# Kernel tuning notes

Measured on AMD Instinct MI355X. Metric: run time of the kernel, lower is better.

## Reference

```python
import jax, jax.numpy as jnp
import numpy as np

N_NODES = 50000
N_EDGES = 1600000
N_GRAPHS = 256
IN_CH = 128
HID = 128
OUT_CH = 10


def gcn_conv(x, W, b, src, dst, ew, num_nodes):
    # PyG GCNConv: add self-loops (weight 1), symmetric deg^-1/2 normalization,
    # linear transform first, aggregate via scatter-add, bias after.
    loop = jnp.arange(num_nodes)
    s = jnp.concatenate([src, loop])
    d = jnp.concatenate([dst, loop])
    w = jnp.concatenate([ew, jnp.ones((num_nodes,), x.dtype)])
    deg = jax.ops.segment_sum(w, d, num_segments=num_nodes)
    dinv = jnp.where(deg > 0, jax.lax.rsqrt(deg), 0.0)
    norm = dinv[s] * dinv[d] * w                     # [E+N]
    h = x @ W                                        # [N, H]
    msg = h[s] * norm[:, None]                       # gather + scale
    out = jax.ops.segment_sum(msg, d, num_segments=num_nodes)  # scatter-add
    return out + b


def setup_inputs() -> dict:
    key = jax.random.key(0)
    ks = jax.random.split(key, 12)
    x = jax.random.normal(ks[0], (N_NODES, IN_CH), jnp.float32)
    edge_index = jax.random.randint(ks[1], (2, N_EDGES), 0, N_NODES, jnp.int64)
    edge_weight = jax.random.uniform(ks[2], (N_EDGES,), jnp.float32)
    batch = jnp.sort(jax.random.randint(ks[3], (N_NODES,), 0, N_GRAPHS, jnp.int64))
    s = 1.0 / np.sqrt(HID)
    W1 = jax.random.normal(ks[4], (IN_CH, HID), jnp.float32) / np.sqrt(IN_CH)
    b1 = jnp.zeros((HID,), jnp.float32)
    W2 = jax.random.normal(ks[5], (HID, HID), jnp.float32) * s
    b2 = jnp.zeros((HID,), jnp.float32)
    W3 = jax.random.normal(ks[6], (HID, HID), jnp.float32) * s
    b3 = jnp.zeros((HID,), jnp.float32)
    lw1 = jax.random.normal(ks[7], (HID, HID), jnp.float32) * s
    lb1 = jax.random.normal(ks[8], (HID,), jnp.float32) * s
    lw2 = jax.random.normal(ks[9], (HID, OUT_CH), jnp.float32) * s
    lb2 = jax.random.normal(ks[10], (OUT_CH,), jnp.float32) * s
    return {"x": x, "edge_index": edge_index, "edge_weight": edge_weight,
            "batch": batch, "W1": W1, "b1": b1, "W2": W2, "b2": b2,
            "W3": W3, "b3": b3, "lw1": lw1, "lb1": lb1, "lw2": lw2, "lb2": lb2}


def reference(x, edge_index, edge_weight, batch, W1, b1, W2, b2, W3, b3, lw1, lb1, lw2, lb2):
    src, dst = edge_index[0], edge_index[1]
    h = jax.nn.relu(gcn_conv(x, W1, b1, src, dst, edge_weight, N_NODES))
    h = jax.nn.relu(gcn_conv(h, W2, b2, src, dst, edge_weight, N_NODES))
    h = gcn_conv(h, W3, b3, src, dst, edge_weight, N_NODES)
    # global mean pool over graphs
    sums = jax.ops.segment_sum(h, batch, num_segments=N_GRAPHS)
    cnt = jax.ops.segment_sum(jnp.ones((N_NODES,), h.dtype), batch, num_segments=N_GRAPHS)
    emb = sums / jnp.maximum(cnt, 1.0)[:, None]      # [G, HID]
    out = (emb @ lw1 + lb1) @ lw2 + lb2              # classify: lin1 -> lin2
    return out
```

## Files before the change

### kernel.cpp

```cpp
#include <hip/hip_runtime.h>

#define N_NODES 50000
#define N_EDGES 1600000
#define N_GRAPHS 256
#define HID 128
#define OUT_CH 10
#define NBUCK 512
#define BNODES ((N_NODES + NBUCK - 1) / NBUCK)
#define BCAP 6144
#define P1BLK 250
#define EPB (N_EDGES / P1BLK)
#define DSENTINEL 127
#define NR 4
#define RSTEP ((N_NODES + NR - 1) / NR)
#define PAD_R 40

typedef __bf16 bf16x8 __attribute__((ext_vector_type(8)));
typedef float f32x4 __attribute__((ext_vector_type(4)));

__device__ inline unsigned bf16rne(float f) {
    unsigned u = __float_as_uint(f);
    return (u + 0x7fffu + ((u >> 16) & 1u)) >> 16;
}

__global__ __launch_bounds__(1024) void bucket_k(const int* __restrict__ src,
                                                 const int* __restrict__ dst,
                                                 const float* __restrict__ ew,
                                                 int* __restrict__ bcount,
                                                 int2* __restrict__ cpair) {
    __shared__ int hist[NBUCK];
    __shared__ int base[NBUCK];
    int t = threadIdx.x;
    for (int i = t; i < NBUCK; i += 1024) hist[i] = 0;
    __syncthreads();
    const int ch0 = blockIdx.x * (EPB / 4);
    const int ch1 = ch0 + (EPB / 4);
    const int4* dst4 = (const int4*)dst;
    for (int ci = ch0 + t; ci < ch1; ci += 1024) {
        int4 d4 = dst4[ci];
        atomicAdd(&hist[d4.x / BNODES], 1);
        atomicAdd(&hist[d4.y / BNODES], 1);
        atomicAdd(&hist[d4.z / BNODES], 1);
        atomicAdd(&hist[d4.w / BNODES], 1);
    }
    __syncthreads();
    for (int i = t; i < NBUCK; i += 1024) {
        int c = hist[i];
        base[i] = (c > 0) ? atomicAdd(&bcount[i], (c + 7) & ~7) : 0;
        hist[i] = 0;
    }
    __syncthreads();
    for (int ci = ch0 + t; ci < ch1; ci += 1024) {
        int4 d4 = dst4[ci];
        int e = ci * 4;
#define PROC(dd, ee)                                              \
        {                                                         \
            int b = (dd) / BNODES;                                \
            int off = base[b] + atomicAdd(&hist[b], 1);           \
            if (off < BCAP) {                                     \
                int2 p;                                           \
                p.x = (((dd) - b * BNODES) << 16) | src[ee];      \
                p.y = __float_as_int(ew[ee]);                     \
                cpair[b * BCAP + off] = p;                        \
            }                                                     \
        }
        PROC(d4.x, e)
        PROC(d4.y, e + 1)
        PROC(d4.z, e + 2)
        PROC(d4.w, e + 3)
#undef PROC
    }
    __syncthreads();
    for (int i = t; i < NBUCK; i += 1024) {
        int c = hist[i];
        int ac = (c + 7) & ~7;
        for (int j = c; j < ac; ++j) {
            int off = base[i] + j;
            if (off < BCAP) {
                int2 p;
                p.x = DSENTINEL << 16;
                p.y = 0;
                cpair[i * BCAP + off] = p;
            }
        }
    }
}

__global__ __launch_bounds__(512) void ell_scatter_k(const int* __restrict__ bcount,
                                                     const int2* __restrict__ cpair,
                                                     int2* __restrict__ ell,
                                                     unsigned* __restrict__ fill4,
                                                     float* __restrict__ dinv) {
    __shared__ int lfill[BNODES * NR];
    __shared__ float wsum[BNODES];
    int b = blockIdx.x;
    int t = threadIdx.x;
    for (int i = t; i < BNODES * NR; i += 512) lfill[i] = 0;
    for (int i = t; i < BNODES; i += 512) wsum[i] = 0.f;
    __syncthreads();
    int cnt = bcount[b];
    if (cnt > BCAP) cnt = BCAP;
    int n0 = b * BNODES;
    int sbase = b * BCAP;
    for (int i = t; i < cnt; i += 512) {
        int2 p = cpair[sbase + i];
        int dloc = p.x >> 16;
        if (dloc < BNODES) {
            int s = p.x & 0xffff;
            int r = s / RSTEP;
            int pos = atomicAdd(&lfill[dloc * NR + r], 1);
            atomicAdd(&wsum[dloc], __int_as_float(p.y));
            if (pos < PAD_R) {
                int2 q;
                q.x = s;
                q.y = p.y;
                ell[((size_t)(n0 + dloc) * NR + r) * PAD_R + pos] = q;
            }
        }
    }
    __syncthreads();
    for (int i = t; i < BNODES; i += 512) {
        int n = n0 + i;
        if (n < N_NODES) {
            unsigned f = 0;
#pragma unroll
            for (int r = 0; r < NR; ++r) {
                int c = lfill[i * NR + r];
                if (c > PAD_R) c = PAD_R;
                f |= (unsigned)c << (8 * r);
            }
            fill4[n] = f;
            dinv[n] = rsqrtf(wsum[i] + 1.0f);
        }
    }
}

__global__ __launch_bounds__(256) void prep_k(const int* __restrict__ batch,
                                              int* __restrict__ gstart,
                                              const float* __restrict__ W1,
                                              const float* __restrict__ W2,
                                              const float* __restrict__ W3,
                                              unsigned short* __restrict__ Wt) {
    int idx = blockIdx.x * 256 + threadIdx.x;
    if (idx < 3 * 16384) {
        int m = idx >> 14;
        int r = idx & 16383;
        const float* W = (m == 0) ? W1 : (m == 1) ? W2 : W3;
        int c = r >> 7, k = r & 127;
        Wt[idx] = (unsigned short)bf16rne(W[k * 128 + c]);
    }
    if (idx < N_NODES) {
        int b = batch[idx];
        int bprev = (idx == 0) ? -1 : batch[idx - 1];
        for (int g = bprev + 1; g <= b; ++g) gstart[g] = idx;
        if (idx == N_NODES - 1) {
            for (int g = b + 1; g <= N_GRAPHS; ++g) gstart[g] = N_NODES;
        }
    }
}

__global__ __launch_bounds__(256) void gemm_mfma_k(const float* __restrict__ A32,
                                                   const unsigned short* __restrict__ Ab,
                                                   const unsigned short* __restrict__ Wt,
                                                   unsigned short* __restrict__ Cb,
                                                   int n_rows) {
    int tid = threadIdx.x;
    int wave = tid >> 6;
    int lane = tid & 63;
    int m = lane & 15;
    int quad = lane >> 4;
    int row = blockIdx.x * 64 + wave * 16 + m;
    int rowc = row < n_rows ? row : n_rows - 1;
    f32x4 acc[8] = {};
#pragma unroll
    for (int kc = 0; kc < 4; ++kc) {
        bf16x8 a;
        if (A32) {
            const float4* Ar = (const float4*)(A32 + (size_t)rowc * 128 + kc * 32 + quad * 8);
            float4 lo = Ar[0], hi = Ar[1];
            union { bf16x8 v; unsigned short s[8]; } u;
            u.s[0] = (unsigned short)bf16rne(lo.x);
            u.s[1] = (unsigned short)bf16rne(lo.y);
            u.s[2] = (unsigned short)bf16rne(lo.z);
            u.s[3] = (unsigned short)bf16rne(lo.w);
            u.s[4] = (unsigned short)bf16rne(hi.x);
            u.s[5] = (unsigned short)bf16rne(hi.y);
            u.s[6] = (unsigned short)bf16rne(hi.z);
            u.s[7] = (unsigned short)bf16rne(hi.w);
            a = u.v;
        } else {
            a = *(const bf16x8*)(Ab + (size_t)rowc * 128 + kc * 32 + quad * 8);
        }
#pragma unroll
        for (int ct = 0; ct < 8; ++ct) {
            bf16x8 b = *(const bf16x8*)(Wt + (size_t)(ct * 16 + m) * 128 + kc * 32 + quad * 8);
            acc[ct] = __builtin_amdgcn_mfma_f32_16x16x32_bf16(a, b, acc[ct], 0, 0, 0);
        }
    }
    int obase = blockIdx.x * 64 + wave * 16 + quad * 4;
#pragma unroll
    for (int ct = 0; ct < 8; ++ct) {
#pragma unroll
        for (int r = 0; r < 4; ++r) {
            int n = obase + r;
            if (n < n_rows)
                Cb[(size_t)n * 128 + ct * 16 + m] = (unsigned short)bf16rne(acc[ct][r]);
        }
    }
}

__global__ __launch_bounds__(256) void agg_k(const unsigned short* __restrict__ tb,
                                             const unsigned* __restrict__ fill4,
                                             const int2* __restrict__ ell,
                                             const float* __restrict__ dinv,
                                             const float* __restrict__ bias,
                                             unsigned short* __restrict__ outB, int relu) {
    int lane = threadIdx.x & 15;
    int local = threadIdx.x >> 4;
    int n = blockIdx.x * 16 + local;
    if (n >= N_NODES) return;
    float dn = dinv[n];
#define UNP(q, f)                                                 \
    float f##0 = __uint_as_float((q).x << 16);                    \
    float f##1 = __uint_as_float((q).x & 0xffff0000u);            \
    float f##2 = __uint_as_float((q).y << 16);                    \
    float f##3 = __uint_as_float((q).y & 0xffff0000u);            \
    float f##4 = __uint_as_float((q).z << 16);                    \
    float f##5 = __uint_as_float((q).z & 0xffff0000u);            \
    float f##6 = __uint_as_float((q).w << 16);                    \
    float f##7 = __uint_as_float((q).w & 0xffff0000u);
    uint4 qs = ((const uint4*)(tb + (size_t)n * 128))[lane];
    UNP(qs, s)
    float acc0 = s0 * dn, acc1 = s1 * dn, acc2 = s2 * dn, acc3 = s3 * dn;
    float acc4 = s4 * dn, acc5 = s5 * dn, acc6 = s6 * dn, acc7 = s7 * dn;
    unsigned f4 = fill4[n];
#pragma unroll
    for (int r = 0; r < NR; ++r) {
        int c = (f4 >> (8 * r)) & 255;
        const int2* ep = ell + ((size_t)n * NR + r) * PAD_R;
        int i = 0;
        for (; i + 4 <= c; i += 4) {
            int2 p0 = ep[i], p1 = ep[i + 1], p2 = ep[i + 2], p3 = ep[i + 3];
            uint4 q0 = ((const uint4*)(tb + (size_t)p0.x * 128))[lane];
            uint4 q1 = ((const uint4*)(tb + (size_t)p1.x * 128))[lane];
            uint4 q2 = ((const uint4*)(tb + (size_t)p2.x * 128))[lane];
            uint4 q3 = ((const uint4*)(tb + (size_t)p3.x * 128))[lane];
            float w0 = __int_as_float(p0.y) * dinv[p0.x];
            float w1 = __int_as_float(p1.y) * dinv[p1.x];
            float w2 = __int_as_float(p2.y) * dinv[p2.x];
            float w3 = __int_as_float(p3.y) * dinv[p3.x];
            UNP(q0, a)
            UNP(q1, b)
            UNP(q2, cc)
            UNP(q3, d)
            acc0 += a0 * w0 + b0 * w1 + cc0 * w2 + d0 * w3;
            acc1 += a1 * w0 + b1 * w1 + cc1 * w2 + d1 * w3;
            acc2 += a2 * w0 + b2 * w1 + cc2 * w2 + d2 * w3;
            acc3 += a3 * w0 + b3 * w1 + cc3 * w2 + d3 * w3;
            acc4 += a4 * w0 + b4 * w1 + cc4 * w2 + d4 * w3;
            acc5 += a5 * w0 + b5 * w1 + cc5 * w2 + d5 * w3;
            acc6 += a6 * w0 + b6 * w1 + cc6 * w2 + d6 * w3;
            acc7 += a7 * w0 + b7 * w1 + cc7 * w2 + d7 * w3;
        }
        for (; i < c; ++i) {
            int2 p = ep[i];
            float w = __int_as_float(p.y) * dinv[p.x];
            uint4 q = ((const uint4*)(tb + (size_t)p.x * 128))[lane];
            UNP(q, a)
            acc0 += a0 * w; acc1 += a1 * w; acc2 += a2 * w; acc3 += a3 * w;
            acc4 += a4 * w; acc5 += a5 * w; acc6 += a6 * w; acc7 += a7 * w;
        }
    }
#undef UNP
    float4 b0 = ((const float4*)bias)[lane * 2];
    float4 b1 = ((const float4*)bias)[lane * 2 + 1];
    acc0 = acc0 * dn + b0.x; acc1 = acc1 * dn + b0.y;
    acc2 = acc2 * dn + b0.z; acc3 = acc3 * dn + b0.w;
    acc4 = acc4 * dn + b1.x; acc5 = acc5 * dn + b1.y;
    acc6 = acc6 * dn + b1.z; acc7 = acc7 * dn + b1.w;
    if (relu) {
        acc0 = fmaxf(acc0, 0.f); acc1 = fmaxf(acc1, 0.f);
        acc2 = fmaxf(acc2, 0.f); acc3 = fmaxf(acc3, 0.f);
        acc4 = fmaxf(acc4, 0.f); acc5 = fmaxf(acc5, 0.f);
        acc6 = fmaxf(acc6, 0.f); acc7 = fmaxf(acc7, 0.f);
    }
    uint4 pk;
    pk.x = bf16rne(acc0) | (bf16rne(acc1) << 16);
    pk.y = bf16rne(acc2) | (bf16rne(acc3) << 16);
    pk.z = bf16rne(acc4) | (bf16rne(acc5) << 16);
    pk.w = bf16rne(acc6) | (bf16rne(acc7) << 16);
    ((uint4*)(outB + (size_t)n * 128))[lane] = pk;
}

#define PCHUNK 49
__global__ __launch_bounds__(128) void pool1_k(const unsigned short* __restrict__ hb,
                                               const int* __restrict__ batch,
                                               float* __restrict__ pool) {
    int c = threadIdx.x;
    int n0 = blockIdx.x * PCHUNK;
    if (n0 >= N_NODES) return;
    int n1 = n0 + PCHUNK;
    if (n1 > N_NODES) n1 = N_NODES;
    int g = batch[n0];
    float run = 0.f;
    for (int n = n0; n < n1; ++n) {
        int gn = batch[n];
        if (gn != g) {
            atomicAdd(&pool[g * 128 + c], run);
            run = 0.f;
            g = gn;
        }
        run += __uint_as_float((unsigned)hb[(size_t)n * 128 + c] << 16);
    }
    atomicAdd(&pool[g * 128 + c], run);
}

__global__ __launch_bounds__(128) void cls2_k(const float* __restrict__ pool,
                                              const int* __restrict__ gstart,
                                              const float* __restrict__ lw1,
                                              const float* __restrict__ lb1,
                                              const float* __restrict__ lw2,
                                              const float* __restrict__ lb2,
                                              float* __restrict__ out) {
    __shared__ float emb[128];
    __shared__ float mid[128];
    int g = blockIdx.x, c = threadIdx.x;
    float cntf = fmaxf((float)(gstart[g + 1] - gstart[g]), 1.0f);
    emb[c] = pool[(size_t)g * 128 + c] / cntf;
    __syncthreads();
    float a = lb1[c];
    for (int k = 0; k < 128; ++k) a += emb[k] * lw1[k * 128 + c];
    mid[c] = a;
    __syncthreads();
    if (c < OUT_CH) {
        float o = lb2[c];
        for (int k = 0; k < 128; ++k) o += mid[k] * lw2[k * OUT_CH + c];
        out[g * OUT_CH + c] = o;
    }
}

extern "C" void kernel_launch(void* const* d_in, const int* in_sizes, int n_in,
                              void* d_out, int out_size, void* d_ws, size_t ws_size,
                              hipStream_t stream) {
    const float* x = (const float*)d_in[0];
    const int* ei = (const int*)d_in[1];
    const int* src = ei;
    const int* dst = ei + N_EDGES;
    const float* ew = (const float*)d_in[2];
    const int* batch = (const int*)d_in[3];
    const float* W1 = (const float*)d_in[4];
    const float* b1 = (const float*)d_in[5];
    const float* W2 = (const float*)d_in[6];
    const float* b2 = (const float*)d_in[7];
    const float* W3 = (const float*)d_in[8];
    const float* b3 = (const float*)d_in[9];
    const float* lw1 = (const float*)d_in[10];
    const float* lb1 = (const float*)d_in[11];
    const float* lw2 = (const float*)d_in[12];
    const float* lb2 = (const float*)d_in[13];
    float* out = (float*)d_out;

    char* ws = (char*)d_ws;
    size_t off = 0;
    auto alloc = [&](size_t bytes) {
        size_t cur = off;
        off += (bytes + 255) & ~(size_t)255;
        return cur;
    };
    size_t o_bcount = alloc(NBUCK * 4);
    size_t o_pool = alloc(N_GRAPHS * HID * 4);
    size_t zero_end = off;
    size_t o_fill4 = alloc(N_NODES * 4);
    size_t o_dinv = alloc(N_NODES * 4);
    size_t o_gstart = alloc((N_GRAPHS + 1) * 4);
    size_t o_wt = alloc(3 * 16384 * 2);
    size_t o_ell = alloc((size_t)N_NODES * NR * PAD_R * 8);
    size_t o_cpair = alloc((size_t)NBUCK * BCAP * 8);
    size_t o_gAb = alloc((size_t)N_NODES * HID * 2);
    size_t o_aggB = alloc((size_t)N_NODES * HID * 2);
    (void)ws_size;

    int* bcount = (int*)(ws + o_bcount);
    float* pool = (float*)(ws + o_pool);
    unsigned* fill4 = (unsigned*)(ws + o_fill4);
    float* dinv = (float*)(ws + o_dinv);
    int* gstart = (int*)(ws + o_gstart);
    unsigned short* Wt = (unsigned short*)(ws + o_wt);
    int2* ell = (int2*)(ws + o_ell);
    int2* cpair = (int2*)(ws + o_cpair);
    unsigned short* gAb = (unsigned short*)(ws + o_gAb);
    unsigned short* aggB = (unsigned short*)(ws + o_aggB);

    hipMemsetAsync(d_ws, 0, zero_end, stream);

    bucket_k<<<P1BLK, 1024, 0, stream>>>(src, dst, ew, bcount, cpair);
    ell_scatter_k<<<NBUCK, 512, 0, stream>>>(bcount, cpair, ell, fill4, dinv);
    prep_k<<<196, 256, 0, stream>>>(batch, gstart, W1, W2, W3, Wt);

    int gemm_blocks = (N_NODES + 63) / 64;
    int agg_blocks = (N_NODES + 15) / 16;
    gemm_mfma_k<<<gemm_blocks, 256, 0, stream>>>(x, (const unsigned short*)0, Wt, gAb, N_NODES);
    agg_k<<<agg_blocks, 256, 0, stream>>>(gAb, fill4, ell, dinv, b1, aggB, 1);
    gemm_mfma_k<<<gemm_blocks, 256, 0, stream>>>((const float*)0, aggB, Wt + 16384, gAb, N_NODES);
    agg_k<<<agg_blocks, 256, 0, stream>>>(gAb, fill4, ell, dinv, b2, aggB, 1);
    gemm_mfma_k<<<gemm_blocks, 256, 0, stream>>>((const float*)0, aggB, Wt + 32768, gAb, N_NODES);
    agg_k<<<agg_blocks, 256, 0, stream>>>(gAb, fill4, ell, dinv, b3, aggB, 0);

    pool1_k<<<(N_NODES + PCHUNK - 1) / PCHUNK, 128, 0, stream>>>(aggB, batch, pool);
    cls2_k<<<N_GRAPHS, 128, 0, stream>>>(pool, gstart, lw1, lb1, lw2, lb2, out);
}
```

Measured before the change: 392.0 us.

## Aggregate before transform and fuse GEMM into aggregation kernel

Reorders each GCN layer to aggregate the raw features first and then apply the weight matrix, using linearity (A·X·W = (A·X)·W). The GEMM is fused into the aggregation kernel through a shared-memory tile and MFMA, and a separate kernel converts x to bf16 once. This drops three standalone GEMM launches and the round trip of the intermediate feature matrix through global memory. In exchange the rounding order changes: features are rounded to bf16 after aggregation instead of after the transform. The fused kernel also carries extra shared-memory and register pressure under a 6-block occupancy hint.

```diff
diff --git a/kernel.cpp b/kernel.cpp
--- a/kernel.cpp
+++ b/kernel.cpp
@@ -159,66 +159,32 @@
     }
 }
 
-__global__ __launch_bounds__(256) void gemm_mfma_k(const float* __restrict__ A32,
-                                                   const unsigned short* __restrict__ Ab,
+__global__ __launch_bounds__(256) void xconv_k(const float* __restrict__ x,
+                                               unsigned short* __restrict__ xb) {
+    int i = blockIdx.x * 256 + threadIdx.x;
+    if (i >= N_NODES * 16) return;
+    const float4* p = (const float4*)x + (size_t)i * 2;
+    float4 lo = p[0], hi = p[1];
+    uint4 pk;
+    pk.x = bf16rne(lo.x) | (bf16rne(lo.y) << 16);
+    pk.y = bf16rne(lo.z) | (bf16rne(lo.w) << 16);
+    pk.z = bf16rne(hi.x) | (bf16rne(hi.y) << 16);
+    pk.w = bf16rne(hi.z) | (bf16rne(hi.w) << 16);
+    ((uint4*)xb)[i] = pk;
+}
+
+__global__ __launch_bounds__(256, 6) void aggemm_k(const unsigned short* __restrict__ tb,
+                                                   const unsigned* __restrict__ fill4,
+                                                   const int2* __restrict__ ell,
+                                                   const float* __restrict__ dinv,
                                                    const unsigned short* __restrict__ Wt,
-                                                   unsigned short* __restrict__ Cb,
-                                                   int n_rows) {
-    int tid = threadIdx.x;
-    int wave = tid >> 6;
-    int lane = tid & 63;
-    int m = lane & 15;
-    int quad = lane >> 4;
-    int row = blockIdx.x * 64 + wave * 16 + m;
-    int rowc = row < n_rows ? row : n_rows - 1;
-    f32x4 acc[8] = {};
-#pragma unroll
-    for (int kc = 0; kc < 4; ++kc) {
-        bf16x8 a;
-        if (A32) {
-            const float4* Ar = (const float4*)(A32 + (size_t)rowc * 128 + kc * 32 + quad * 8);
-            float4 lo = Ar[0], hi = Ar[1];
-            union { bf16x8 v; unsigned short s[8]; } u;
-            u.s[0] = (unsigned short)bf16rne(lo.x);
-            u.s[1] = (unsigned short)bf16rne(lo.y);
-            u.s[2] = (unsigned short)bf16rne(lo.z);
-            u.s[3] = (unsigned short)bf16rne(lo.w);
-            u.s[4] = (unsigned short)bf16rne(hi.x);
-            u.s[5] = (unsigned short)bf16rne(hi.y);
-            u.s[6] = (unsigned short)bf16rne(hi.z);
-            u.s[7] = (unsigned short)bf16rne(hi.w);
-            a = u.v;
-        } else {
-            a = *(const bf16x8*)(Ab + (size_t)rowc * 128 + kc * 32 + quad * 8);
-        }
-#pragma unroll
-        for (int ct = 0; ct < 8; ++ct) {
-            bf16x8 b = *(const bf16x8*)(Wt + (size_t)(ct * 16 + m) * 128 + kc * 32 + quad * 8);
-            acc[ct] = __builtin_amdgcn_mfma_f32_16x16x32_bf16(a, b, acc[ct], 0, 0, 0);
-        }
-    }
-    int obase = blockIdx.x * 64 + wave * 16 + quad * 4;
-#pragma unroll
-    for (int ct = 0; ct < 8; ++ct) {
-#pragma unroll
-        for (int r = 0; r < 4; ++r) {
-            int n = obase + r;
-            if (n < n_rows)
-                Cb[(size_t)n * 128 + ct * 16 + m] = (unsigned short)bf16rne(acc[ct][r]);
-        }
-    }
-}
-
-__global__ __launch_bounds__(256) void agg_k(const unsigned short* __restrict__ tb,
-                                             const unsigned* __restrict__ fill4,
-                                             const int2* __restrict__ ell,
-                                             const float* __restrict__ dinv,
-                                             const float* __restrict__ bias,
-                                             unsigned short* __restrict__ outB, int relu) {
-    int lane = threadIdx.x & 15;
+                                                   const float* __restrict__ bias,
+                                                   unsigned short* __restrict__ outB,
+                                                   int relu) {
+    __shared__ unsigned short tile[16][136];
+    int lane16 = threadIdx.x & 15;
     int local = threadIdx.x >> 4;
     int n = blockIdx.x * 16 + local;
-    if (n >= N_NODES) return;
     float dn = dinv[n];
 #define UNP(q, f)                                                 \
     float f##0 = __uint_as_float((q).x << 16);                    \
@@ -229,7 +195,7 @@
     float f##5 = __uint_as_float((q).z & 0xffff0000u);            \
     float f##6 = __uint_as_float((q).w << 16);                    \
     float f##7 = __uint_as_float((q).w & 0xffff0000u);
-    uint4 qs = ((const uint4*)(tb + (size_t)n * 128))[lane];
+    uint4 qs = ((const uint4*)(tb + (size_t)n * 128))[lane16];
     UNP(qs, s)
     float acc0 = s0 * dn, acc1 = s1 * dn, acc2 = s2 * dn, acc3 = s3 * dn;
     float acc4 = s4 * dn, acc5 = s5 * dn, acc6 = s6 * dn, acc7 = s7 * dn;
@@ -241,10 +207,10 @@
         int i = 0;
         for (; i + 4 <= c; i += 4) {
             int2 p0 = ep[i], p1 = ep[i + 1], p2 = ep[i + 2], p3 = ep[i + 3];
-            uint4 q0 = ((const uint4*)(tb + (size_t)p0.x * 128))[lane];
-            uint4 q1 = ((const uint4*)(tb + (size_t)p1.x * 128))[lane];
-            uint4 q2 = ((const uint4*)(tb + (size_t)p2.x * 128))[lane];
-            uint4 q3 = ((const uint4*)(tb + (size_t)p3.x * 128))[lane];
+            uint4 q0 = ((const uint4*)(tb + (size_t)p0.x * 128))[lane16];
+            uint4 q1 = ((const uint4*)(tb + (size_t)p1.x * 128))[lane16];
+            uint4 q2 = ((const uint4*)(tb + (size_t)p2.x * 128))[lane16];
+            uint4 q3 = ((const uint4*)(tb + (size_t)p3.x * 128))[lane16];
             float w0 = __int_as_float(p0.y) * dinv[p0.x];
             float w1 = __int_as_float(p1.y) * dinv[p1.x];
             float w2 = __int_as_float(p2.y) * dinv[p2.x];
@@ -265,31 +231,50 @@
         for (; i < c; ++i) {
             int2 p = ep[i];
             float w = __int_as_float(p.y) * dinv[p.x];
-            uint4 q = ((const uint4*)(tb + (size_t)p.x * 128))[lane];
+            uint4 q = ((const uint4*)(tb + (size_t)p.x * 128))[lane16];
             UNP(q, a)
             acc0 += a0 * w; acc1 += a1 * w; acc2 += a2 * w; acc3 += a3 * w;
             acc4 += a4 * w; acc5 += a5 * w; acc6 += a6 * w; acc7 += a7 * w;
         }
     }
 #undef UNP
-    float4 b0 = ((const float4*)bias)[lane * 2];
-    float4 b1 = ((const float4*)bias)[lane * 2 + 1];
-    acc0 = acc0 * dn + b0.x; acc1 = acc1 * dn + b0.y;
-    acc2 = acc2 * dn + b0.z; acc3 = acc3 * dn + b0.w;
-    acc4 = acc4 * dn + b1.x; acc5 = acc5 * dn + b1.y;
-    acc6 = acc6 * dn + b1.z; acc7 = acc7 * dn + b1.w;
-    if (relu) {
-        acc0 = fmaxf(acc0, 0.f); acc1 = fmaxf(acc1, 0.f);
-        acc2 = fmaxf(acc2, 0.f); acc3 = fmaxf(acc3, 0.f);
-        acc4 = fmaxf(acc4, 0.f); acc5 = fmaxf(acc5, 0.f);
-        acc6 = fmaxf(acc6, 0.f); acc7 = fmaxf(acc7, 0.f);
-    }
+    acc0 *= dn; acc1 *= dn; acc2 *= dn; acc3 *= dn;
+    acc4 *= dn; acc5 *= dn; acc6 *= dn; acc7 *= dn;
     uint4 pk;
     pk.x = bf16rne(acc0) | (bf16rne(acc1) << 16);
     pk.y = bf16rne(acc2) | (bf16rne(acc3) << 16);
     pk.z = bf16rne(acc4) | (bf16rne(acc5) << 16);
     pk.w = bf16rne(acc6) | (bf16rne(acc7) << 16);
-    ((uint4*)(outB + (size_t)n * 128))[lane] = pk;
+    *(uint4*)&tile[local][lane16 * 8] = pk;
+    __syncthreads();
+
+    int wave = threadIdx.x >> 6;
+    int lane = threadIdx.x & 63;
+    int m = lane & 15;
+    int quad = lane >> 4;
+    f32x4 acc[2] = {};
+#pragma unroll
+    for (int kc = 0; kc < 4; ++kc) {
+        bf16x8 a = *(const bf16x8*)&tile[m][kc * 32 + quad * 8];
+#pragma unroll
+        for (int ctl = 0; ctl < 2; ++ctl) {
+            int ct = wave * 2 + ctl;
+            bf16x8 bfr = *(const bf16x8*)(Wt + (size_t)(ct * 16 + m) * 128 + kc * 32 + quad * 8);
+            acc[ctl] = __builtin_amdgcn_mfma_f32_16x16x32_bf16(a, bfr, acc[ctl], 0, 0, 0);
+        }
+    }
+#pragma unroll
+    for (int ctl = 0; ctl < 2; ++ctl) {
+        int col = (wave * 2 + ctl) * 16 + m;
+        float bv = bias[col];
+#pragma unroll
+        for (int r = 0; r < 4; ++r) {
+            int nr = blockIdx.x * 16 + quad * 4 + r;
+            float v = acc[ctl][r] + bv;
+            if (relu) v = fmaxf(v, 0.f);
+            outB[(size_t)nr * 128 + col] = (unsigned short)bf16rne(v);
+        }
+    }
 }
 
 #define PCHUNK 49
@@ -376,8 +361,8 @@
     size_t o_wt = alloc(3 * 16384 * 2);
     size_t o_ell = alloc((size_t)N_NODES * NR * PAD_R * 8);
     size_t o_cpair = alloc((size_t)NBUCK * BCAP * 8);
-    size_t o_gAb = alloc((size_t)N_NODES * HID * 2);
-    size_t o_aggB = alloc((size_t)N_NODES * HID * 2);
+    size_t o_featA = alloc((size_t)N_NODES * HID * 2);
+    size_t o_featB = alloc((size_t)N_NODES * HID * 2);
     (void)ws_size;
 
     int* bcount = (int*)(ws + o_bcount);
@@ -388,24 +373,21 @@
     unsigned short* Wt = (unsigned short*)(ws + o_wt);
     int2* ell = (int2*)(ws + o_ell);
     int2* cpair = (int2*)(ws + o_cpair);
-    unsigned short* gAb = (unsigned short*)(ws + o_gAb);
-    unsigned short* aggB = (unsigned short*)(ws + o_aggB);
+    unsigned short* featA = (unsigned short*)(ws + o_featA);
+    unsigned short* featB = (unsigned short*)(ws + o_featB);
 
     hipMemsetAsync(d_ws, 0, zero_end, stream);
 
     bucket_k<<<P1BLK, 1024, 0, stream>>>(src, dst, ew, bcount, cpair);
     ell_scatter_k<<<NBUCK, 512, 0, stream>>>(bcount, cpair, ell, fill4, dinv);
     prep_k<<<196, 256, 0, stream>>>(batch, gstart, W1, W2, W3, Wt);
-
-    int gemm_blocks = (N_NODES + 63) / 64;
+    xconv_k<<<(N_NODES * 16 + 255) / 256, 256, 0, stream>>>(x, featA);
+
     int agg_blocks = (N_NODES + 15) / 16;
-    gemm_mfma_k<<<gemm_blocks, 256, 0, stream>>>(x, (const unsigned short*)0, Wt, gAb, N_NODES);
-    agg_k<<<agg_blocks, 256, 0, stream>>>(gAb, fill4, ell, dinv, b1, aggB, 1);
-    gemm_mfma_k<<<gemm_blocks, 256, 0, stream>>>((const float*)0, aggB, Wt + 16384, gAb, N_NODES);
-    agg_k<<<agg_blocks, 256, 0, stream>>>(gAb, fill4, ell, dinv, b2, aggB, 1);
-    gemm_mfma_k<<<gemm_blocks, 256, 0, stream>>>((const float*)0, aggB, Wt + 32768, gAb, N_NODES);
-    agg_k<<<agg_blocks, 256, 0, stream>>>(gAb, fill4, ell, dinv, b3, aggB, 0);
-
-    pool1_k<<<(N_NODES + PCHUNK - 1) / PCHUNK, 128, 0, stream>>>(aggB, batch, pool);
+    aggemm_k<<<agg_blocks, 256, 0, stream>>>(featA, fill4, ell, dinv, Wt, b1, featB, 1);
+    aggemm_k<<<agg_blocks, 256, 0, stream>>>(featB, fill4, ell, dinv, Wt + 16384, b2, featA, 1);
+    aggemm_k<<<agg_blocks, 256, 0, stream>>>(featA, fill4, ell, dinv, Wt + 32768, b3, featB, 0);
+
+    pool1_k<<<(N_NODES + PCHUNK - 1) / PCHUNK, 128, 0, stream>>>(featB, batch, pool);
     cls2_k<<<N_GRAPHS, 128, 0, stream>>>(pool, gstart, lw1, lb1, lw2, lb2, out);
 }
```

Measured after the change: 358.9 us. 1.09x faster.
